# Performance work log

Measured on AMD Instinct MI355X. Metric: run time of the kernel, lower is better.

The kernel has to match this reference:

```python
import jax, jax.numpy as jnp
import numpy as np

EPS = 1e-5

def layer_norm(x, g, b):
    mu = jnp.mean(x, axis=-1, keepdims=True)
    var = jnp.var(x, axis=-1, keepdims=True)
    return (x - mu) * jax.lax.rsqrt(var + EPS) * g + b

def setup_inputs() -> dict:
    key = jax.random.key(0)
    ks = jax.random.split(key, 16)
    N, E, D, ED = 50000, 500000, 128, 5
    def w(k, i, o):
        return jax.random.normal(k, (i, o), jnp.float32) / np.sqrt(i)
    return {
        "x": jax.random.normal(ks[0], (N, D), jnp.float32),
        "edge_attr": jax.random.normal(ks[1], (E, ED), jnp.float32),
        "pos": jax.random.normal(ks[2], (N, 3), jnp.float32),
        "node_w1": w(ks[3], D, D), "node_b1": jnp.zeros((D,), jnp.float32),
        "node_g1": jnp.ones((D,), jnp.float32), "node_be1": jnp.zeros((D,), jnp.float32),
        "node_w2": w(ks[4], D, D), "node_b2": jnp.zeros((D,), jnp.float32),
        "edge_w1": w(ks[5], 2 * D + ED, D), "edge_b1": jnp.zeros((D,), jnp.float32),
        "edge_g1": jnp.ones((D,), jnp.float32), "edge_be1": jnp.zeros((D,), jnp.float32),
        "edge_w2": w(ks[6], D, D), "edge_b2": jnp.zeros((D,), jnp.float32),
        "upd_w": w(ks[7], 2 * D, D), "upd_b": jnp.zeros((D,), jnp.float32),
        "ln_g": jnp.ones((D,), jnp.float32), "ln_b": jnp.zeros((D,), jnp.float32),
        "edge_index": jax.random.randint(ks[8], (2, E), 0, N, jnp.int64),
    }

def reference(x, edge_attr, pos, node_w1, node_b1, node_g1, node_be1, node_w2, node_b2,
              edge_w1, edge_b1, edge_g1, edge_be1, edge_w2, edge_b2,
              upd_w, upd_b, ln_g, ln_b, edge_index):
    N = x.shape[0]
    # node MLP: Linear -> LayerNorm -> ReLU -> Linear (dropout=0)
    h_nodes = jax.nn.relu(layer_norm(x @ node_w1 + node_b1, node_g1, node_be1)) @ node_w2 + node_b2
    src, dst = edge_index[0], edge_index[1]
    # edge MLP on gathered endpoint features + edge_attr  [E, 2D+edge_dim]
    ef = jnp.concatenate([x[src], x[dst], edge_attr], axis=1)
    h_edges = jax.nn.relu(layer_norm(ef @ edge_w1 + edge_b1, edge_g1, edge_be1)) @ edge_w2 + edge_b2
    # scatter-add aggregation to destination nodes
    h_agg = jax.ops.segment_sum(h_edges, dst, num_segments=N)
    h_out = jnp.concatenate([h_nodes, h_agg], axis=1) @ upd_w + upd_b
    h_out = h_out + x  # residual (in_channels == out_channels)
    return layer_norm(h_out, ln_g, ln_b)
```

## Files before the change

### kernel.cpp

```cpp
#include <hip/hip_runtime.h>
#include <stdint.h>

#define D    128
#define ED   5
#define BLK  512
#define WPB  8
#define W1S  296
#define W2S  136
#define HS   136
#define US   264
#define GRID 256

typedef __attribute__((ext_vector_type(8))) short bf16x8;
typedef __attribute__((ext_vector_type(4))) float f32x4;

__device__ __forceinline__ unsigned short f2bf(float f) {
    union { float f; uint32_t u; } c; c.f = f;
    uint32_t r = (c.u + 0x7fffu + ((c.u >> 16) & 1u)) >> 16;
    return (unsigned short)r;
}
__device__ __forceinline__ float bflo(uint32_t u) {
    union { uint32_t u; float f; } c; c.u = u << 16; return c.f;
}
__device__ __forceinline__ float bfhi(uint32_t u) {
    union { uint32_t u; float f; } c; c.u = u & 0xffff0000u; return c.f;
}
__device__ __forceinline__ bf16x8 cvt8(const float* __restrict__ p) {
    float4 a = *(const float4*)p;
    float4 b = *(const float4*)(p + 4);
    bf16x8 r;
    r[0] = (short)f2bf(a.x); r[1] = (short)f2bf(a.y);
    r[2] = (short)f2bf(a.z); r[3] = (short)f2bf(a.w);
    r[4] = (short)f2bf(b.x); r[5] = (short)f2bf(b.y);
    r[6] = (short)f2bf(b.z); r[7] = (short)f2bf(b.w);
    return r;
}
__device__ __forceinline__ bool detect64(const int* ei) {
    return (ei[1] == 0) & (ei[3] == 0) & (ei[5] == 0) &
           (ei[7] == 0) & (ei[9] == 0) & (ei[11] == 0);
}

__global__ __launch_bounds__(512)
void cvt_count_kernel(const float* __restrict__ in, unsigned short* __restrict__ out,
                      int n8, const int* __restrict__ ei, int* __restrict__ cnt, int E) {
    const int i = blockIdx.x * 512 + threadIdx.x;
    if (i < n8) {
        float4 a = ((const float4*)in)[2 * i];
        float4 b = ((const float4*)in)[2 * i + 1];
        union { unsigned short s[8]; uint4 v; } p;
        p.s[0] = f2bf(a.x); p.s[1] = f2bf(a.y); p.s[2] = f2bf(a.z); p.s[3] = f2bf(a.w);
        p.s[4] = f2bf(b.x); p.s[5] = f2bf(b.y); p.s[6] = f2bf(b.z); p.s[7] = f2bf(b.w);
        ((uint4*)out)[i] = p.v;
    } else {
        const int e = i - n8;
        if (e < E) {
            const bool is64 = detect64(ei);
            int d = is64 ? ei[2 * ((size_t)E + e)] : ei[(size_t)E + e];
            atomicAdd(&cnt[d], 1);
        }
    }
}

__global__ __launch_bounds__(1024)
void scan_blk_kernel(const int* __restrict__ cnt, int* __restrict__ part,
                     int* __restrict__ bsum, int N) {
    __shared__ int wsum[16];
    const int tid = threadIdx.x, wave = tid >> 6, lane = tid & 63;
    const int idx = blockIdx.x * 1024 + tid;
    int v = (idx < N) ? cnt[idx] : 0;
    int s = v;
    #pragma unroll
    for (int off = 1; off < 64; off <<= 1) {
        int t = __shfl_up(s, off, 64);
        if (lane >= off) s += t;
    }
    if (lane == 63) wsum[wave] = s;
    __syncthreads();
    if (wave == 0 && lane < 16) {
        int ws_ = wsum[lane];
        #pragma unroll
        for (int off = 1; off < 16; off <<= 1) {
            int t = __shfl_up(ws_, off, 64);
            if (lane >= off) ws_ += t;
        }
        wsum[lane] = ws_;
    }
    __syncthreads();
    const int excl = ((wave == 0) ? 0 : wsum[wave - 1]) + (s - v);
    if (idx < N) part[idx] = excl;
    if (tid == 0) bsum[blockIdx.x] = wsum[15];
}

__global__ __launch_bounds__(1024)
void scan_top_kernel(int* __restrict__ bsum, int nb) {
    __shared__ int wsum[16];
    const int tid = threadIdx.x, wave = tid >> 6, lane = tid & 63;
    int v = (tid < nb) ? bsum[tid] : 0;
    int s = v;
    #pragma unroll
    for (int off = 1; off < 64; off <<= 1) {
        int t = __shfl_up(s, off, 64);
        if (lane >= off) s += t;
    }
    if (lane == 63) wsum[wave] = s;
    __syncthreads();
    if (wave == 0 && lane < 16) {
        int ws_ = wsum[lane];
        #pragma unroll
        for (int off = 1; off < 16; off <<= 1) {
            int t = __shfl_up(ws_, off, 64);
            if (lane >= off) ws_ += t;
        }
        wsum[lane] = ws_;
    }
    __syncthreads();
    const int excl = ((wave == 0) ? 0 : wsum[wave - 1]) + (s - v);
    if (tid < nb) bsum[tid] = excl;
}

__global__ __launch_bounds__(1024)
void scan_add_kernel(const int* __restrict__ part, const int* __restrict__ bsum,
                     int* __restrict__ starts, int* __restrict__ cursor,
                     int N, int E) {
    const int idx = blockIdx.x * 1024 + threadIdx.x;
    if (idx < N) {
        int v = part[idx] + bsum[blockIdx.x];
        starts[idx] = v;
        cursor[idx] = v;
    }
    if (blockIdx.x == 0 && threadIdx.x == 0) starts[N] = E;
}

__global__ __launch_bounds__(512)
void fill_kernel(const int* __restrict__ ei, int* __restrict__ cursor,
                 int* __restrict__ eids, int E) {
    const bool is64 = detect64(ei);
    int e = blockIdx.x * 512 + threadIdx.x;
    if (e >= E) return;
    int d = is64 ? ei[2 * ((size_t)E + e)] : ei[(size_t)E + e];
    int pos = atomicAdd(&cursor[d], 1);
    eids[pos] = e;
}

__global__ __launch_bounds__(512)
void agg_kernel(const unsigned short* __restrict__ h2, const int* __restrict__ starts,
                unsigned short* __restrict__ aggb, int N) {
    const int wid = blockIdx.x * WPB + (threadIdx.x >> 6);
    if (wid >= N) return;
    const int lane = threadIdx.x & 63;
    const int s = starts[wid], t = starts[wid + 1];
    const unsigned short* p = h2 + (size_t)s * D + 2 * lane;
    const int n = t - s;
    float a0 = 0.f, a1 = 0.f, b0 = 0.f, b1 = 0.f;
    float p0 = 0.f, p1 = 0.f, q0 = 0.f, q1 = 0.f;
    int j = 0;
    for (; j + 4 <= n; j += 4) {
        uint32_t u0 = *(const uint32_t*)(p + (size_t)(j + 0) * D);
        uint32_t u1 = *(const uint32_t*)(p + (size_t)(j + 1) * D);
        uint32_t u2 = *(const uint32_t*)(p + (size_t)(j + 2) * D);
        uint32_t u3 = *(const uint32_t*)(p + (size_t)(j + 3) * D);
        a0 += bflo(u0); a1 += bfhi(u0);
        b0 += bflo(u1); b1 += bfhi(u1);
        p0 += bflo(u2); p1 += bfhi(u2);
        q0 += bflo(u3); q1 += bfhi(u3);
    }
    for (; j < n; ++j) {
        uint32_t u = *(const uint32_t*)(p + (size_t)j * D);
        a0 += bflo(u); a1 += bfhi(u);
    }
    const float r0 = (a0 + b0) + (p0 + q0);
    const float r1 = (a1 + b1) + (p1 + q1);
    uint32_t o = (uint32_t)f2bf(r0) | ((uint32_t)f2bf(r1) << 16);
    *(uint32_t*)(aggb + (size_t)wid * D + 2 * lane) = o;
}

template<bool EDGE, bool XBF, bool CSR>
__global__ __launch_bounds__(BLK, 2)
void mlp_kernel(const float* __restrict__ x, const unsigned short* __restrict__ xbf,
                const float* __restrict__ ea, const int* __restrict__ ei,
                const int* __restrict__ eids,
                const float* __restrict__ w1, const float* __restrict__ b1,
                const float* __restrict__ g1, const float* __restrict__ be1,
                const float* __restrict__ w2, const float* __restrict__ b2,
                unsigned short* __restrict__ hout, float* __restrict__ aggf,
                int N, int E)
{
    __shared__ unsigned short w1t[128 * W1S];
    __shared__ unsigned short w2t[128 * W2S];
    __shared__ unsigned short hb[WPB][16 * HS];

    const int tid = threadIdx.x;
    const int KROWS = EDGE ? 288 : 128;
    for (int i = tid; i < KROWS * 128; i += BLK) {
        int k = i >> 7, n = i & 127;
        float v = (!EDGE || k < (2 * D + ED)) ? w1[k * 128 + n] : 0.f;
        w1t[n * W1S + k] = f2bf(v);
    }
    for (int i = tid; i < 128 * 128; i += BLK) {
        int k = i >> 7, n = i & 127;
        w2t[n * W2S + k] = f2bf(w2[k * 128 + n]);
    }
    __syncthreads();

    bool is64 = false;
    if (EDGE) is64 = detect64(ei);

    const int lane = tid & 63, w = tid >> 6;
    const int g = lane >> 4, c = lane & 15;

    float b1v[8], g1v[8], e1v[8], b2v[8];
    #pragma unroll
    for (int nt = 0; nt < 8; ++nt) {
        b1v[nt] = b1[nt * 16 + c];  g1v[nt] = g1[nt * 16 + c];
        e1v[nt] = be1[nt * 16 + c]; b2v[nt] = b2[nt * 16 + c];
    }

    const int cnt = EDGE ? E : N;
    const int nT = (cnt + 15) >> 4;
    const int step = gridDim.x * WPB;
    unsigned short* hw = hb[w];

    int pdd = 0, pe = 0;
    size_t paoff = 0, pboff = 0;
    bf16x8 pf[9];

    auto loadIdx = [&](int tl) {
        const int rr = tl * 16 + c;
        const int rc = rr < cnt ? rr : cnt - 1;
        if (EDGE) {
            const int e = CSR ? eids[rc] : rc;
            pe = e;
            int s = is64 ? ei[2 * (size_t)e]       : ei[e];
            pdd   = is64 ? ei[2 * ((size_t)E + e)] : ei[(size_t)E + e];
            paoff = (size_t)s * D;
            pboff = (size_t)pdd * D;
        } else {
            pe = rc;
            paoff = (size_t)rc * D;
        }
    };
    auto loadFrags = [&]() {
        #pragma unroll
        for (int kk = 0; kk < (EDGE ? 8 : 4); ++kk) {
            const size_t o = (kk < 4) ? paoff + kk * 32 : pboff + (kk - 4) * 32;
            if (XBF) pf[kk] = *(const bf16x8*)(xbf + o + 8 * g);
            else     pf[kk] = cvt8(x + o + 8 * g);
        }
        if (EDGE) {
            bf16x8 t;
            #pragma unroll
            for (int j = 0; j < 8; ++j) t[j] = 0;
            if (g == 0) {
                #pragma unroll
                for (int j = 0; j < ED; ++j)
                    t[j] = (short)f2bf(ea[(size_t)pe * ED + j]);
            }
            pf[8] = t;
        }
    };

    int tile = blockIdx.x * WPB + w;
    if (tile < nT) { loadIdx(tile); loadFrags(); }

    for (; tile < nT; tile += step) {
        bf16x8 af[9];
        #pragma unroll
        for (int kk = 0; kk < (EDGE ? 9 : 4); ++kk) af[kk] = pf[kk];
        const int dd = pdd;
        const int row = tile * 16 + c;

        const int tn = tile + step;
        loadIdx(tn < nT ? tn : tile);

        const f32x4 z = {0.f, 0.f, 0.f, 0.f};
        f32x4 acc[8] = {z, z, z, z, z, z, z, z};
        #pragma unroll
        for (int kk = 0; kk < (EDGE ? 9 : 4); ++kk) {
            const unsigned short* wr = &w1t[c * W1S + kk * 32 + 8 * g];
            #pragma unroll
            for (int nt = 0; nt < 8; ++nt) {
                bf16x8 bf = *(const bf16x8*)(wr + nt * 16 * W1S);
                acc[nt] = __builtin_amdgcn_mfma_f32_16x16x32_bf16(af[kk], bf, acc[nt], 0, 0, 0);
            }
        }

        loadFrags();

        float mean[4], rstd[4];
        #pragma unroll
        for (int r = 0; r < 4; ++r) {
            float s = 0.f, q = 0.f;
            #pragma unroll
            for (int nt = 0; nt < 8; ++nt) {
                float v = acc[nt][r] + b1v[nt];
                acc[nt][r] = v;
                s += v; q += v * v;
            }
            s += __shfl_xor(s, 1, 64); q += __shfl_xor(q, 1, 64);
            s += __shfl_xor(s, 2, 64); q += __shfl_xor(q, 2, 64);
            s += __shfl_xor(s, 4, 64); q += __shfl_xor(q, 4, 64);
            s += __shfl_xor(s, 8, 64); q += __shfl_xor(q, 8, 64);
            float m = s * (1.f / 128.f);
            float var = q * (1.f / 128.f) - m * m;
            mean[r] = m;
            rstd[r] = rsqrtf(var + 1e-5f);
        }
        #pragma unroll
        for (int nt = 0; nt < 8; ++nt) {
            #pragma unroll
            for (int r = 0; r < 4; ++r) {
                float h = fmaxf((acc[nt][r] - mean[r]) * rstd[r] * g1v[nt] + e1v[nt], 0.f);
                hw[(4 * g + r) * HS + nt * 16 + c] = f2bf(h);
            }
        }

        f32x4 acc2[8] = {z, z, z, z, z, z, z, z};
        #pragma unroll
        for (int kk = 0; kk < 4; ++kk) {
            bf16x8 hf = *(const bf16x8*)&hw[c * HS + kk * 32 + 8 * g];
            const unsigned short* wr = &w2t[c * W2S + kk * 32 + 8 * g];
            #pragma unroll
            for (int nt = 0; nt < 8; ++nt) {
                bf16x8 bf = *(const bf16x8*)(wr + nt * 16 * W2S);
                acc2[nt] = __builtin_amdgcn_mfma_f32_16x16x32_bf16(hf, bf, acc2[nt], 0, 0, 0);
            }
        }

        if (EDGE && !CSR) {
            int dv[4];
            #pragma unroll
            for (int r = 0; r < 4; ++r) dv[r] = __shfl(dd, 4 * g + r, 64);
            #pragma unroll
            for (int r = 0; r < 4; ++r) {
                const int er = tile * 16 + 4 * g + r;
                if (er < cnt) {
                    float* dst = aggf + (size_t)dv[r] * D + c;
                    #pragma unroll
                    for (int nt = 0; nt < 8; ++nt)
                        atomicAdd(dst + nt * 16, acc2[nt][r] + b2v[nt]);
                }
            }
        } else {
            #pragma unroll
            for (int nt = 0; nt < 8; ++nt) {
                #pragma unroll
                for (int r = 0; r < 4; ++r)
                    hw[(4 * g + r) * HS + nt * 16 + c] = f2bf(acc2[nt][r] + b2v[nt]);
            }
            if (row < cnt) {
                unsigned short* dst = hout + (size_t)row * D;
                #pragma unroll
                for (int j = 0; j < 4; ++j)
                    *(uint4*)(dst + (j * 4 + g) * 8) =
                        *(const uint4*)&hw[c * HS + (j * 4 + g) * 8];
            }
        }
    }
}

template<bool AGGBF, bool XBF>
__global__ __launch_bounds__(BLK, 4)
void upd2_kernel(const unsigned short* __restrict__ hnb, const void* __restrict__ aggp,
                 const float* __restrict__ x, const unsigned short* __restrict__ xbf,
                 const float* __restrict__ uw, const float* __restrict__ ub,
                 const float* __restrict__ lg, const float* __restrict__ lb,
                 float* __restrict__ out, int N)
{
    __shared__ unsigned short wt[128 * US];
    const int tid = threadIdx.x;
    for (int i = tid; i < 256 * 128; i += BLK) {
        int k = i >> 7, n = i & 127;
        wt[n * US + k] = f2bf(uw[i]);
    }
    __syncthreads();

    const int lane = tid & 63, w = tid >> 6;
    const int g = lane >> 4, c = lane & 15;

    float ubv[8], gv[8], bv[8];
    #pragma unroll
    for (int nt = 0; nt < 8; ++nt) {
        ubv[nt] = ub[nt * 16 + c]; gv[nt] = lg[nt * 16 + c]; bv[nt] = lb[nt * 16 + c];
    }

    const int nT = (N + 15) >> 4;
    for (int tile = blockIdx.x * WPB + w; tile < nT; tile += gridDim.x * WPB) {
        const int row = tile * 16 + c;
        const int rc  = row < N ? row : N - 1;

        const f32x4 z = {0.f, 0.f, 0.f, 0.f};
        f32x4 acc[8] = {z, z, z, z, z, z, z, z};

        #pragma unroll
        for (int kk = 0; kk < 8; ++kk) {
            bf16x8 af;
            if (kk < 4) {
                af = *(const bf16x8*)(hnb + (size_t)rc * D + kk * 32 + 8 * g);
            } else {
                if (AGGBF)
                    af = *(const bf16x8*)((const unsigned short*)aggp +
                                          (size_t)rc * D + (kk - 4) * 32 + 8 * g);
                else
                    af = cvt8((const float*)aggp + (size_t)rc * D + (kk - 4) * 32 + 8 * g);
            }
            const unsigned short* wr = &wt[c * US + kk * 32 + 8 * g];
            #pragma unroll
            for (int nt = 0; nt < 8; ++nt) {
                bf16x8 bf = *(const bf16x8*)(wr + nt * 16 * US);
                acc[nt] = __builtin_amdgcn_mfma_f32_16x16x32_bf16(af, bf, acc[nt], 0, 0, 0);
            }
        }

        float mean[4], rstd[4];
        #pragma unroll
        for (int r = 0; r < 4; ++r) {
            const int row4 = tile * 16 + 4 * g + r;
            const int r4c = row4 < N ? row4 : N - 1;
            float s = 0.f, q = 0.f;
            #pragma unroll
            for (int nt = 0; nt < 8; ++nt) {
                float xr;
                if (XBF) xr = bflo((uint32_t)xbf[(size_t)r4c * D + nt * 16 + c]);
                else     xr = x[(size_t)r4c * D + nt * 16 + c];
                float v = acc[nt][r] + ubv[nt] + xr;
                acc[nt][r] = v;
                s += v; q += v * v;
            }
            s += __shfl_xor(s, 1, 64); q += __shfl_xor(q, 1, 64);
            s += __shfl_xor(s, 2, 64); q += __shfl_xor(q, 2, 64);
            s += __shfl_xor(s, 4, 64); q += __shfl_xor(q, 4, 64);
            s += __shfl_xor(s, 8, 64); q += __shfl_xor(q, 8, 64);
            float m = s * (1.f / 128.f);
            mean[r] = m;
            rstd[r] = rsqrtf(q * (1.f / 128.f) - m * m + 1e-5f);
        }
        #pragma unroll
        for (int r = 0; r < 4; ++r) {
            const int row4 = tile * 16 + 4 * g + r;
            if (row4 < N) {
                #pragma unroll
                for (int nt = 0; nt < 8; ++nt)
                    out[(size_t)row4 * D + nt * 16 + c] =
                        (acc[nt][r] - mean[r]) * rstd[r] * gv[nt] + bv[nt];
            }
        }
    }
}

extern "C" void kernel_launch(void* const* d_in, const int* in_sizes, int n_in,
                              void* d_out, int out_size, void* d_ws, size_t ws_size,
                              hipStream_t stream)
{
    const float* x    = (const float*)d_in[0];
    const float* ea   = (const float*)d_in[1];
    const float* nw1  = (const float*)d_in[3];
    const float* nb1  = (const float*)d_in[4];
    const float* ng1  = (const float*)d_in[5];
    const float* nbe1 = (const float*)d_in[6];
    const float* nw2  = (const float*)d_in[7];
    const float* nb2  = (const float*)d_in[8];
    const float* ew1  = (const float*)d_in[9];
    const float* eb1  = (const float*)d_in[10];
    const float* eg1  = (const float*)d_in[11];
    const float* ebe1 = (const float*)d_in[12];
    const float* ew2  = (const float*)d_in[13];
    const float* eb2  = (const float*)d_in[14];
    const float* uw   = (const float*)d_in[15];
    const float* ub   = (const float*)d_in[16];
    const float* lg   = (const float*)d_in[17];
    const float* lb   = (const float*)d_in[18];
    const int*   eidx = (const int*)d_in[19];

    const int N = in_sizes[0] / D;
    const int E = in_sizes[1] / ED;

    char* base = (char*)d_ws;
    size_t off = 0;
    auto alloc = [&](size_t bytes) -> char* {
        char* p = base + off;
        off = (off + bytes + 255) & ~(size_t)255;
        return p;
    };

    unsigned short* hnb  = (unsigned short*)alloc((size_t)N * D * 2);
    unsigned short* aggb = (unsigned short*)alloc((size_t)N * D * 2);
    unsigned short* xbf  = (unsigned short*)alloc((size_t)N * D * 2);
    int* cnt    = (int*)alloc((size_t)N * 4);
    int* starts = (int*)alloc(((size_t)N + 1) * 4);
    int* cursor = (int*)alloc((size_t)N * 4);
    int* bsum   = (int*)alloc(1024 * 4);
    int* eids   = (int*)alloc((size_t)E * 4);
    unsigned short* h2 = (unsigned short*)alloc((size_t)E * D * 2);
    const size_t needA = off;

    const int n8 = N * D / 8;
    const int egrid = (E + 511) / 512;
    const int nb = (N + 1023) / 1024;
    const int ugrid = (((N + 15) / 16) + WPB - 1) / WPB;

    if (ws_size >= needA && nb <= 1024) {
        hipMemsetAsync(cnt, 0, (size_t)N * 4, stream);
        cvt_count_kernel<<<(n8 + E + 511) / 512, 512, 0, stream>>>(
            x, xbf, n8, eidx, cnt, E);
        scan_blk_kernel<<<nb, 1024, 0, stream>>>(cnt, cursor, bsum, N);
        scan_top_kernel<<<1, 1024, 0, stream>>>(bsum, nb);
        scan_add_kernel<<<nb, 1024, 0, stream>>>(cursor, bsum, starts, cursor, N, E);
        fill_kernel<<<egrid, 512, 0, stream>>>(eidx, cursor, eids, E);
        mlp_kernel<false, true, true><<<GRID, BLK, 0, stream>>>(
            x, xbf, nullptr, nullptr, nullptr, nw1, nb1, ng1, nbe1, nw2, nb2,
            hnb, nullptr, N, E);
        mlp_kernel<true, true, true><<<GRID, BLK, 0, stream>>>(
            x, xbf, ea, eidx, eids, ew1, eb1, eg1, ebe1, ew2, eb2,
            h2, nullptr, N, E);
        agg_kernel<<<(N + WPB - 1) / WPB, 512, 0, stream>>>(h2, starts, aggb, N);
        upd2_kernel<true, true><<<ugrid, BLK, 0, stream>>>(
            hnb, aggb, x, xbf, uw, ub, lg, lb, (float*)d_out, N);
        return;
    }

    off = 0;
    unsigned short* hnb2 = (unsigned short*)alloc((size_t)N * D * 2);
    float* aggf = (float*)alloc((size_t)N * D * 4);
    unsigned short* xbf2 = (unsigned short*)alloc((size_t)N * D * 2);
    const size_t needB = off;

    hipMemsetAsync(aggf, 0, (size_t)N * D * 4, stream);
    if (ws_size >= needB) {
        cvt_count_kernel<<<(n8 + 511) / 512, 512, 0, stream>>>(
            x, xbf2, n8, nullptr, nullptr, 0);
        mlp_kernel<false, true, false><<<GRID, BLK, 0, stream>>>(
            x, xbf2, nullptr, nullptr, nullptr, nw1, nb1, ng1, nbe1, nw2, nb2,
            hnb2, nullptr, N, E);
        mlp_kernel<true, true, false><<<GRID, BLK, 0, stream>>>(
            x, xbf2, ea, eidx, nullptr, ew1, eb1, eg1, ebe1, ew2, eb2,
            nullptr, aggf, N, E);
        upd2_kernel<false, true><<<ugrid, BLK, 0, stream>>>(
            hnb2, aggf, x, xbf2, uw, ub, lg, lb, (float*)d_out, N);
    } else {
        mlp_kernel<false, false, false><<<GRID, BLK, 0, stream>>>(
            x, nullptr, nullptr, nullptr, nullptr, nw1, nb1, ng1, nbe1, nw2, nb2,
            hnb2, nullptr, N, E);
        mlp_kernel<true, false, false><<<GRID, BLK, 0, stream>>>(
            x, nullptr, ea, eidx, nullptr, ew1, eb1, eg1, ebe1, ew2, eb2,
            nullptr, aggf, N, E);
        upd2_kernel<false, false><<<ugrid, BLK, 0, stream>>>(
            hnb2, aggf, x, nullptr, uw, ub, lg, lb, (float*)d_out, N);
    }
}
```

Measured before the change: 472.1 us.

## Fuse CSR aggregation into update kernel and scatter edge outputs by slot

The edge MLP now reads edges in original order, which gives coalesced edge_index and edge_attr reads, and writes each output row to its CSR slot computed by fill_kernel. The separate aggregation kernel and its bf16 intermediate buffer are removed. The update kernel sums each node's contiguous h2 rows directly in registers before the MFMA. The risk is load imbalance, because each lane loops over its own node's degree, and the h2 writes become scattered.

```diff
diff --git a/kernel.cpp b/kernel.cpp
--- a/kernel.cpp
+++ b/kernel.cpp
@@ -133,52 +133,19 @@
 
 __global__ __launch_bounds__(512)
 void fill_kernel(const int* __restrict__ ei, int* __restrict__ cursor,
-                 int* __restrict__ eids, int E) {
+                 int* __restrict__ slotp, int E) {
     const bool is64 = detect64(ei);
     int e = blockIdx.x * 512 + threadIdx.x;
     if (e >= E) return;
     int d = is64 ? ei[2 * ((size_t)E + e)] : ei[(size_t)E + e];
-    int pos = atomicAdd(&cursor[d], 1);
-    eids[pos] = e;
-}
-
-__global__ __launch_bounds__(512)
-void agg_kernel(const unsigned short* __restrict__ h2, const int* __restrict__ starts,
-                unsigned short* __restrict__ aggb, int N) {
-    const int wid = blockIdx.x * WPB + (threadIdx.x >> 6);
-    if (wid >= N) return;
-    const int lane = threadIdx.x & 63;
-    const int s = starts[wid], t = starts[wid + 1];
-    const unsigned short* p = h2 + (size_t)s * D + 2 * lane;
-    const int n = t - s;
-    float a0 = 0.f, a1 = 0.f, b0 = 0.f, b1 = 0.f;
-    float p0 = 0.f, p1 = 0.f, q0 = 0.f, q1 = 0.f;
-    int j = 0;
-    for (; j + 4 <= n; j += 4) {
-        uint32_t u0 = *(const uint32_t*)(p + (size_t)(j + 0) * D);
-        uint32_t u1 = *(const uint32_t*)(p + (size_t)(j + 1) * D);
-        uint32_t u2 = *(const uint32_t*)(p + (size_t)(j + 2) * D);
-        uint32_t u3 = *(const uint32_t*)(p + (size_t)(j + 3) * D);
-        a0 += bflo(u0); a1 += bfhi(u0);
-        b0 += bflo(u1); b1 += bfhi(u1);
-        p0 += bflo(u2); p1 += bfhi(u2);
-        q0 += bflo(u3); q1 += bfhi(u3);
-    }
-    for (; j < n; ++j) {
-        uint32_t u = *(const uint32_t*)(p + (size_t)j * D);
-        a0 += bflo(u); a1 += bfhi(u);
-    }
-    const float r0 = (a0 + b0) + (p0 + q0);
-    const float r1 = (a1 + b1) + (p1 + q1);
-    uint32_t o = (uint32_t)f2bf(r0) | ((uint32_t)f2bf(r1) << 16);
-    *(uint32_t*)(aggb + (size_t)wid * D + 2 * lane) = o;
+    slotp[e] = atomicAdd(&cursor[d], 1);
 }
 
 template<bool EDGE, bool XBF, bool CSR>
 __global__ __launch_bounds__(BLK, 2)
 void mlp_kernel(const float* __restrict__ x, const unsigned short* __restrict__ xbf,
                 const float* __restrict__ ea, const int* __restrict__ ei,
-                const int* __restrict__ eids,
+                const int* __restrict__ slotp,
                 const float* __restrict__ w1, const float* __restrict__ b1,
                 const float* __restrict__ g1, const float* __restrict__ be1,
                 const float* __restrict__ w2, const float* __restrict__ b2,
@@ -220,22 +187,21 @@
     const int step = gridDim.x * WPB;
     unsigned short* hw = hb[w];
 
-    int pdd = 0, pe = 0;
+    int pdd = 0, prc = 0, psl = 0;
     size_t paoff = 0, pboff = 0;
     bf16x8 pf[9];
 
     auto loadIdx = [&](int tl) {
         const int rr = tl * 16 + c;
         const int rc = rr < cnt ? rr : cnt - 1;
+        prc = rc;
         if (EDGE) {
-            const int e = CSR ? eids[rc] : rc;
-            pe = e;
-            int s = is64 ? ei[2 * (size_t)e]       : ei[e];
-            pdd   = is64 ? ei[2 * ((size_t)E + e)] : ei[(size_t)E + e];
+            int s = is64 ? ei[2 * (size_t)rc]       : ei[rc];
+            pdd   = is64 ? ei[2 * ((size_t)E + rc)] : ei[(size_t)E + rc];
             paoff = (size_t)s * D;
             pboff = (size_t)pdd * D;
+            if (CSR) psl = slotp[rc];
         } else {
-            pe = rc;
             paoff = (size_t)rc * D;
         }
     };
@@ -253,7 +219,7 @@
             if (g == 0) {
                 #pragma unroll
                 for (int j = 0; j < ED; ++j)
-                    t[j] = (short)f2bf(ea[(size_t)pe * ED + j]);
+                    t[j] = (short)f2bf(ea[(size_t)prc * ED + j]);
             }
             pf[8] = t;
         }
@@ -267,6 +233,7 @@
         #pragma unroll
         for (int kk = 0; kk < (EDGE ? 9 : 4); ++kk) af[kk] = pf[kk];
         const int dd = pdd;
+        const int sl = psl;
         const int row = tile * 16 + c;
 
         const int tn = tile + step;
@@ -348,11 +315,119 @@
                     hw[(4 * g + r) * HS + nt * 16 + c] = f2bf(acc2[nt][r] + b2v[nt]);
             }
             if (row < cnt) {
-                unsigned short* dst = hout + (size_t)row * D;
+                const int orow = (EDGE && CSR) ? sl : row;
+                unsigned short* dst = hout + (size_t)orow * D;
                 #pragma unroll
                 for (int j = 0; j < 4; ++j)
                     *(uint4*)(dst + (j * 4 + g) * 8) =
                         *(const uint4*)&hw[c * HS + (j * 4 + g) * 8];
+            }
+        }
+    }
+}
+
+template<bool XBF>
+__global__ __launch_bounds__(BLK, 2)
+void upd3_kernel(const unsigned short* __restrict__ hnb,
+                 const unsigned short* __restrict__ h2, const int* __restrict__ starts,
+                 const float* __restrict__ x, const unsigned short* __restrict__ xbf,
+                 const float* __restrict__ uw, const float* __restrict__ ub,
+                 const float* __restrict__ lg, const float* __restrict__ lb,
+                 float* __restrict__ out, int N)
+{
+    __shared__ unsigned short wt[128 * US];
+    const int tid = threadIdx.x;
+    for (int i = tid; i < 256 * 128; i += BLK) {
+        int k = i >> 7, n = i & 127;
+        wt[n * US + k] = f2bf(uw[i]);
+    }
+    __syncthreads();
+
+    const int lane = tid & 63, w = tid >> 6;
+    const int g = lane >> 4, c = lane & 15;
+
+    float ubv[8], gv[8], bv[8];
+    #pragma unroll
+    for (int nt = 0; nt < 8; ++nt) {
+        ubv[nt] = ub[nt * 16 + c]; gv[nt] = lg[nt * 16 + c]; bv[nt] = lb[nt * 16 + c];
+    }
+
+    const int nT = (N + 15) >> 4;
+    for (int tile = blockIdx.x * WPB + w; tile < nT; tile += gridDim.x * WPB) {
+        const int row = tile * 16 + c;
+        const int rc  = row < N ? row : N - 1;
+
+        const int s = starts[rc], t = starts[rc + 1];
+        float ag0[8] = {0,0,0,0,0,0,0,0}, ag1[8] = {0,0,0,0,0,0,0,0};
+        float ag2[8] = {0,0,0,0,0,0,0,0}, ag3[8] = {0,0,0,0,0,0,0,0};
+        for (int j = s; j < t; ++j) {
+            const unsigned short* pr = h2 + (size_t)j * D + 8 * g;
+            uint4 v0 = *(const uint4*)(pr);
+            uint4 v1 = *(const uint4*)(pr + 32);
+            uint4 v2 = *(const uint4*)(pr + 64);
+            uint4 v3 = *(const uint4*)(pr + 96);
+            ag0[0] += bflo(v0.x); ag0[1] += bfhi(v0.x); ag0[2] += bflo(v0.y); ag0[3] += bfhi(v0.y);
+            ag0[4] += bflo(v0.z); ag0[5] += bfhi(v0.z); ag0[6] += bflo(v0.w); ag0[7] += bfhi(v0.w);
+            ag1[0] += bflo(v1.x); ag1[1] += bfhi(v1.x); ag1[2] += bflo(v1.y); ag1[3] += bfhi(v1.y);
+            ag1[4] += bflo(v1.z); ag1[5] += bfhi(v1.z); ag1[6] += bflo(v1.w); ag1[7] += bfhi(v1.w);
+            ag2[0] += bflo(v2.x); ag2[1] += bfhi(v2.x); ag2[2] += bflo(v2.y); ag2[3] += bfhi(v2.y);
+            ag2[4] += bflo(v2.z); ag2[5] += bfhi(v2.z); ag2[6] += bflo(v2.w); ag2[7] += bfhi(v2.w);
+            ag3[0] += bflo(v3.x); ag3[1] += bfhi(v3.x); ag3[2] += bflo(v3.y); ag3[3] += bfhi(v3.y);
+            ag3[4] += bflo(v3.z); ag3[5] += bfhi(v3.z); ag3[6] += bflo(v3.w); ag3[7] += bfhi(v3.w);
+        }
+
+        const f32x4 z = {0.f, 0.f, 0.f, 0.f};
+        f32x4 acc[8] = {z, z, z, z, z, z, z, z};
+
+        #pragma unroll
+        for (int kk = 0; kk < 8; ++kk) {
+            bf16x8 af;
+            if (kk < 4) {
+                af = *(const bf16x8*)(hnb + (size_t)rc * D + kk * 32 + 8 * g);
+            } else {
+                const float* agp = (kk == 4) ? ag0 : (kk == 5) ? ag1 : (kk == 6) ? ag2 : ag3;
+                #pragma unroll
+                for (int i = 0; i < 8; ++i) af[i] = (short)f2bf(agp[i]);
+            }
+            const unsigned short* wr = &wt[c * US + kk * 32 + 8 * g];
+            #pragma unroll
+            for (int nt = 0; nt < 8; ++nt) {
+                bf16x8 bf = *(const bf16x8*)(wr + nt * 16 * US);
+                acc[nt] = __builtin_amdgcn_mfma_f32_16x16x32_bf16(af, bf, acc[nt], 0, 0, 0);
+            }
+        }
+
+        float mean[4], rstd[4];
+        #pragma unroll
+        for (int r = 0; r < 4; ++r) {
+            const int row4 = tile * 16 + 4 * g + r;
+            const int r4c = row4 < N ? row4 : N - 1;
+            float s2 = 0.f, q = 0.f;
+            #pragma unroll
+            for (int nt = 0; nt < 8; ++nt) {
+                float xr;
+                if (XBF) xr = bflo((uint32_t)xbf[(size_t)r4c * D + nt * 16 + c]);
+                else     xr = x[(size_t)r4c * D + nt * 16 + c];
+                float v = acc[nt][r] + ubv[nt] + xr;
+                acc[nt][r] = v;
+                s2 += v; q += v * v;
+            }
+            s2 += __shfl_xor(s2, 1, 64); q += __shfl_xor(q, 1, 64);
+            s2 += __shfl_xor(s2, 2, 64); q += __shfl_xor(q, 2, 64);
+            s2 += __shfl_xor(s2, 4, 64); q += __shfl_xor(q, 4, 64);
+            s2 += __shfl_xor(s2, 8, 64); q += __shfl_xor(q, 8, 64);
+            float m = s2 * (1.f / 128.f);
+            mean[r] = m;
+            rstd[r] = rsqrtf(q * (1.f / 128.f) - m * m + 1e-5f);
+        }
+        #pragma unroll
+        for (int r = 0; r < 4; ++r) {
+            const int row4 = tile * 16 + 4 * g + r;
+            if (row4 < N) {
+                #pragma unroll
+                for (int nt = 0; nt < 8; ++nt)
+                    out[(size_t)row4 * D + nt * 16 + c] =
+                        (acc[nt][r] - mean[r]) * rstd[r] * gv[nt] + bv[nt];
             }
         }
     }
@@ -483,13 +558,12 @@
     };
 
     unsigned short* hnb  = (unsigned short*)alloc((size_t)N * D * 2);
-    unsigned short* aggb = (unsigned short*)alloc((size_t)N * D * 2);
     unsigned short* xbf  = (unsigned short*)alloc((size_t)N * D * 2);
     int* cnt    = (int*)alloc((size_t)N * 4);
     int* starts = (int*)alloc(((size_t)N + 1) * 4);
     int* cursor = (int*)alloc((size_t)N * 4);
     int* bsum   = (int*)alloc(1024 * 4);
-    int* eids   = (int*)alloc((size_t)E * 4);
+    int* slotA  = (int*)alloc((size_t)E * 4);
     unsigned short* h2 = (unsigned short*)alloc((size_t)E * D * 2);
     const size_t needA = off;
 
@@ -505,16 +579,15 @@
         scan_blk_kernel<<<nb, 1024, 0, stream>>>(cnt, cursor, bsum, N);
         scan_top_kernel<<<1, 1024, 0, stream>>>(bsum, nb);
         scan_add_kernel<<<nb, 1024, 0, stream>>>(cursor, bsum, starts, cursor, N, E);
-        fill_kernel<<<egrid, 512, 0, stream>>>(eidx, cursor, eids, E);
+        fill_kernel<<<egrid, 512, 0, stream>>>(eidx, cursor, slotA, E);
         mlp_kernel<false, true, true><<<GRID, BLK, 0, stream>>>(
             x, xbf, nullptr, nullptr, nullptr, nw1, nb1, ng1, nbe1, nw2, nb2,
             hnb, nullptr, N, E);
         mlp_kernel<true, true, true><<<GRID, BLK, 0, stream>>>(
-            x, xbf, ea, eidx, eids, ew1, eb1, eg1, ebe1, ew2, eb2,
+            x, xbf, ea, eidx, slotA, ew1, eb1, eg1, ebe1, ew2, eb2,
             h2, nullptr, N, E);
-        agg_kernel<<<(N + WPB - 1) / WPB, 512, 0, stream>>>(h2, starts, aggb, N);
-        upd2_kernel<true, true><<<ugrid, BLK, 0, stream>>>(
-            hnb, aggb, x, xbf, uw, ub, lg, lb, (float*)d_out, N);
+        upd3_kernel<true><<<ugrid, BLK, 0, stream>>>(
+            hnb, h2, starts, x, xbf, uw, ub, lg, lb, (float*)d_out, N);
         return;
     }
 
```

Result: faster. 410.0 us (-13.1%).
